# Performance work log

Hardware: AMD Instinct MI355X
Metric: run time of the kernel (lower is better)

Reference implementation:

```python
import jax, jax.numpy as jnp
import numpy as np

# Config from module init / global Args
H = 8        # n_head
DK = 64      # d_k
DV = 64      # d_v
D = 512      # d_model
KSZ = 3      # kernel_size (args.kernel_size)
B_PARAM = 0.001
CUR_HEAD = 3
ALPHA_C = -float(np.log(B_PARAM / (H - 1) * CUR_HEAD))  # alpha_c (nonzero head)
EPS = 1e-6


def setup_inputs() -> dict:
    key = jax.random.key(0)
    ks = jax.random.split(key, 8)
    B, L = 2, 2048
    q = jax.random.normal(ks[0], (B, L, D), jnp.float32)
    k = jax.random.normal(ks[1], (B, L, D), jnp.float32)
    v = jax.random.normal(ks[2], (B, L, D), jnp.float32)
    # Linear weights stored torch-style: [out_features, in_features]
    w_q = jax.random.normal(ks[3], (H * DK, D), jnp.float32) * 0.02
    w_k = jax.random.normal(ks[4], (H * DK, D), jnp.float32) * 0.02
    w_v = jax.random.normal(ks[5], (H * DV, D), jnp.float32) * 0.02
    w_fc = jax.random.normal(ks[6], (D, H * DV), jnp.float32) * 0.02
    gamma = jnp.ones((D,), jnp.float32)
    beta = jnp.zeros((D,), jnp.float32)
    return {"q": q, "k": k, "v": v, "w_q": w_q, "w_k": w_k, "w_v": w_v,
            "w_fc": w_fc, "gamma": gamma, "beta": beta}


def reference(q, k, v, w_q, w_k, w_v, w_fc, gamma, beta):
    B, L, _ = q.shape
    residual = q
    # QKV projections -> [B, H, L, d]
    qh = jnp.einsum('bld,ed->ble', q, w_q).reshape(B, L, H, DK).transpose(0, 2, 1, 3)
    kh = jnp.einsum('bld,ed->ble', k, w_k).reshape(B, L, H, DK).transpose(0, 2, 1, 3)
    vh = jnp.einsum('bld,ed->ble', v, w_v).reshape(B, L, H, DV).transpose(0, 2, 1, 3)
    # Scores: matmul(q / sqrt(d_k), k^T)  (LaSAttention receives d_k = d_k**0.5)
    attn = jnp.einsum('bhqd,bhkd->bhqk', qh, kh) / jnp.sqrt(jnp.float32(DK))
    # Distance weighting: eld = alpha_c * -(x - y) * attn, d_l[i,j] = j - i
    idx = jnp.arange(L)
    d_l = idx[None, :] - idx[:, None]                      # [L, L]
    eld_mat = (-ALPHA_C * d_l).astype(attn.dtype)
    eld = eld_mat[None, None, :, :] * attn
    # Softmax then avg_pool1d(kernel=KSZ, stride=1, pad=(KSZ-1)//2, count_include_pad)
    p = jax.nn.softmax(eld, axis=-1)                       # [B, H, L, L]
    pad = (KSZ - 1) // 2
    pp = jnp.pad(p, ((0, 0), (0, 0), (0, 0), (pad, pad)))
    pooled = sum(pp[..., j:j + L] for j in range(KSZ)) / jnp.float32(KSZ)
    # Value matmul (seq lengths equal so no trimming needed)
    out = jnp.einsum('bhqk,bhkd->bhqd', pooled, vh)
    out = out.transpose(0, 2, 1, 3).reshape(B, L, H * DV)
    # Output projection (dropout is identity in eval), residual, LayerNorm
    out = jnp.einsum('ble,de->bld', out, w_fc)
    out = out[:, :, None, :] + residual[:, :, None, :]     # [B, L, 1, D]
    mu = out.mean(axis=-1, keepdims=True)
    var = ((out - mu) ** 2).mean(axis=-1, keepdims=True)
    out = (out - mu) / jnp.sqrt(var + EPS) * gamma + beta
    return (out, pooled)
```

## Files before the change

kernel.cpp:

```cpp
#include <hip/hip_runtime.h>
#include <cstddef>
#include <cstdint>

#define ALPHA_C 7.7550531393693407f
constexpr int BB = 2;
constexpr int LL = 2048;
constexpr int HH = 8;
constexpr size_t OUT0  = (size_t)BB * LL * 512;
constexpr size_t PLANE = (size_t)BB * HH * LL * 64;
constexpr size_t XN    = (size_t)BB * LL * 512;
constexpr size_t WN    = (size_t)512 * 512;
constexpr size_t UN    = (size_t)16 * 32 * 32 * 4096;

typedef __attribute__((ext_vector_type(8))) short bf16x8;
typedef __attribute__((ext_vector_type(4))) short short4v;
typedef __attribute__((ext_vector_type(4))) float f32x4;

__device__ inline short f2bf(float x) {
  union { float f; unsigned u; } un; un.f = x;
  unsigned r = un.u + 0x7fffu + ((un.u >> 16) & 1u);
  return (short)(r >> 16);
}
__device__ inline float bf2f(short s) {
  union { unsigned u; float f; } un; un.u = ((unsigned)(unsigned short)s) << 16;
  return un.f;
}
__device__ inline void split3(float x, short& h, short& m, short& l) {
  h = f2bf(x); float r = x - bf2f(h);
  m = f2bf(r); float r2 = r - bf2f(m);
  l = f2bf(r2);
}

__global__ __launch_bounds__(256) void k_split3x(
    const float* __restrict__ a, const float* __restrict__ b, const float* __restrict__ c,
    short* __restrict__ da, short* __restrict__ db, short* __restrict__ dc, size_t n)
{
  size_t i = ((size_t)blockIdx.x * 256 + threadIdx.x) * 4;
  if (i >= n) return;
  const float* srcs[3] = {a, b, c};
  short* dsts[3] = {da, db, dc};
  #pragma unroll
  for (int s = 0; s < 3; ++s) {
    float4 x = *(const float4*)&srcs[s][i];
    short4v h, m, l;
    short th, tm, tl;
    split3(x.x, th, tm, tl); h[0] = th; m[0] = tm; l[0] = tl;
    split3(x.y, th, tm, tl); h[1] = th; m[1] = tm; l[1] = tl;
    split3(x.z, th, tm, tl); h[2] = th; m[2] = tm; l[2] = tl;
    split3(x.w, th, tm, tl); h[3] = th; m[3] = tm; l[3] = tl;
    *(short4v*)&dsts[s][i]         = h;
    *(short4v*)&dsts[s][n + i]     = m;
    *(short4v*)&dsts[s][2 * n + i] = l;
  }
}

__global__ __launch_bounds__(256) void k_cvtbf(
    const float* __restrict__ src, short* __restrict__ dst, size_t n)
{
  size_t i = ((size_t)blockIdx.x * 256 + threadIdx.x) * 8;
  if (i >= n) return;
  float4 a = *(const float4*)&src[i];
  float4 b = *(const float4*)&src[i + 4];
  bf16x8 o;
  o[0] = f2bf(a.x); o[1] = f2bf(a.y); o[2] = f2bf(a.z); o[3] = f2bf(a.w);
  o[4] = f2bf(b.x); o[5] = f2bf(b.y); o[6] = f2bf(b.z); o[7] = f2bf(b.w);
  *(bf16x8*)&dst[i] = o;
}

__global__ __launch_bounds__(256) void k_vavg(
    const short* __restrict__ vt, short* __restrict__ vavgt)
{
  const size_t row = blockIdx.x;
  const short* src = vt + row * LL;
  short* dst = vavgt + row * LL;
  const int c0 = threadIdx.x * 8;
  bf16x8 x = *(const bf16x8*)&src[c0];
  float xf[10];
  xf[0] = (c0 > 0) ? bf2f(src[c0 - 1]) : 0.f;
  #pragma unroll
  for (int i = 0; i < 8; ++i) xf[i + 1] = bf2f(x[i]);
  xf[9] = (c0 + 8 < LL) ? bf2f(src[c0 + 8]) : 0.f;
  bf16x8 o;
  #pragma unroll
  for (int i = 0; i < 8; ++i) o[i] = f2bf((xf[i] + xf[i + 1] + xf[i + 2]) * (1.0f / 3.0f));
  *(bf16x8*)&dst[c0] = o;
}

__global__ __launch_bounds__(256) void k_proj(
    const short* __restrict__ xq, const short* __restrict__ xk, const short* __restrict__ xv,
    const short* __restrict__ wq3, const short* __restrict__ wk3, const short* __restrict__ wv3,
    short* __restrict__ qs, short* __restrict__ ks, short* __restrict__ vt)
{
  const int bx  = blockIdx.x;
  const int sel = bx >> 3;
  const int n0  = (bx & 7) * 64;
  const int m0  = blockIdx.y * 64;
  const short* X = sel == 0 ? xq  : (sel == 1 ? xk  : xv);
  const short* W = sel == 0 ? wq3 : (sel == 1 ? wk3 : wv3);

  __shared__ short Xs[3][64 * 72];
  __shared__ short Ws[3][64 * 72];
  const int tid = threadIdx.x;
  const int lane = tid & 63, w = tid >> 6;
  const int quad = lane >> 4, l15 = lane & 15, colg = l15;
  const int sr8 = tid >> 3, sc8 = (tid & 7) * 8;

  f32x4 acc[4];
  #pragma unroll
  for (int t = 0; t < 4; ++t) { acc[t][0]=0.f; acc[t][1]=0.f; acc[t][2]=0.f; acc[t][3]=0.f; }

  for (int kt = 0; kt < 8; ++kt) {
    const int k0 = kt * 64;
    #pragma unroll
    for (int p = 0; p < 3; ++p) {
      #pragma unroll
      for (int it = 0; it < 2; ++it) {
        int r = it * 32 + sr8;
        *(bf16x8*)&Xs[p][r * 72 + sc8] = *(const bf16x8*)&X[p * XN + (size_t)(m0 + r) * 512 + k0 + sc8];
        *(bf16x8*)&Ws[p][r * 72 + sc8] = *(const bf16x8*)&W[p * WN + (size_t)(n0 + r) * 512 + k0 + sc8];
      }
    }
    __syncthreads();
    #pragma unroll
    for (int ch = 0; ch < 2; ++ch) {
      const int ka = (quad << 3) + ch * 32;
      const int ar = (w * 16 + l15) * 72 + ka;
      bf16x8 ah = *(const bf16x8*)&Xs[0][ar];
      bf16x8 am = *(const bf16x8*)&Xs[1][ar];
      bf16x8 al = *(const bf16x8*)&Xs[2][ar];
      #pragma unroll
      for (int t = 0; t < 4; ++t) {
        const int br = (t * 16 + l15) * 72 + ka;
        bf16x8 bh_ = *(const bf16x8*)&Ws[0][br];
        bf16x8 bm_ = *(const bf16x8*)&Ws[1][br];
        bf16x8 bl_ = *(const bf16x8*)&Ws[2][br];
        acc[t] = __builtin_amdgcn_mfma_f32_16x16x32_bf16(ah, bh_, acc[t], 0, 0, 0);
        acc[t] = __builtin_amdgcn_mfma_f32_16x16x32_bf16(ah, bm_, acc[t], 0, 0, 0);
        acc[t] = __builtin_amdgcn_mfma_f32_16x16x32_bf16(am, bh_, acc[t], 0, 0, 0);
        acc[t] = __builtin_amdgcn_mfma_f32_16x16x32_bf16(ah, bl_, acc[t], 0, 0, 0);
        acc[t] = __builtin_amdgcn_mfma_f32_16x16x32_bf16(al, bh_, acc[t], 0, 0, 0);
        acc[t] = __builtin_amdgcn_mfma_f32_16x16x32_bf16(am, bm_, acc[t], 0, 0, 0);
      }
    }
    __syncthreads();
  }

  if (sel < 2) {
    short* Y = sel == 0 ? qs : ks;
    #pragma unroll
    for (int t = 0; t < 4; ++t) {
      const int e = n0 + t * 16 + colg, h = e >> 6, dk = e & 63;
      #pragma unroll
      for (int r = 0; r < 4; ++r) {
        const int m = m0 + w * 16 + quad * 4 + r;
        const int b = m >> 11, l = m & 2047;
        size_t base = ((size_t)(b * HH + h) * LL + l) * 64 + dk;
        short hh, mm, ll; split3(acc[t][r], hh, mm, ll);
        Y[base] = hh; Y[PLANE + base] = mm; Y[2 * PLANE + base] = ll;
      }
    }
  } else {
    const int b  = m0 >> 11;
    const int l0 = (m0 & 2047) + w * 16 + quad * 4;
    #pragma unroll
    for (int t = 0; t < 4; ++t) {
      const int e = n0 + t * 16 + colg, h = e >> 6, dk = e & 63;
      short4v s;
      #pragma unroll
      for (int r = 0; r < 4; ++r) s[r] = f2bf(acc[t][r]);
      *(short4v*)&vt[(((size_t)b * HH + h) * 64 + dk) * LL + l0] = s;
    }
  }
}

__global__ __launch_bounds__(256) void k_qk_exp(
    const short* __restrict__ qs, const short* __restrict__ ks,
    short* __restrict__ u_g, float* __restrict__ mstats, float* __restrict__ rowstats)
{
  const int i0 = blockIdx.x * 64;
  const int bh = blockIdx.y;
  __shared__ short Ks[3][64 * 72];
  __shared__ short Us[64 * 72];
  const int tid = threadIdx.x;
  const int lane = tid & 63, w = tid >> 6;
  const int quad = lane >> 4, colg = lane & 15, l15 = lane & 15;
  const int sr8 = tid >> 3, sc8 = (tid & 7) * 8;

  bf16x8 qf[3][2];
  {
    const size_t qoff = ((size_t)bh * LL + i0 + w * 16 + l15) * 64 + (quad << 3);
    #pragma unroll
    for (int p = 0; p < 3; ++p)
      #pragma unroll
      for (int ch = 0; ch < 2; ++ch)
        qf[p][ch] = *(const bf16x8*)&qs[p * PLANE + qoff + ch * 32];
  }

  const short* kbase = ks + (size_t)bh * LL * 64;
  #pragma unroll
  for (int p = 0; p < 3; ++p)
    #pragma unroll
    for (int it = 0; it < 2; ++it) {
      int r = it * 32 + sr8;
      *(bf16x8*)&Ks[p][r * 72 + sc8] = *(const bf16x8*)&kbase[p * PLANE + (size_t)r * 64 + sc8];
    }
  __syncthreads();

  float M[4], S[4];
  #pragma unroll
  for (int r = 0; r < 4; ++r) { M[r] = -3.0e38f; S[r] = 0.f; }

  for (int jt = 0; jt < 32; ++jt) {
    const int j0 = jt * 64;
    bf16x8 kreg[3][2];
    if (jt + 1 < 32) {
      #pragma unroll
      for (int p = 0; p < 3; ++p)
        #pragma unroll
        for (int it = 0; it < 2; ++it) {
          int r = it * 32 + sr8;
          kreg[p][it] = *(const bf16x8*)&kbase[p * PLANE + ((size_t)(jt + 1) * 64 + r) * 64 + sc8];
        }
    }

    f32x4 acc[4];
    #pragma unroll
    for (int t = 0; t < 4; ++t) { acc[t][0]=0.f; acc[t][1]=0.f; acc[t][2]=0.f; acc[t][3]=0.f; }
    #pragma unroll
    for (int ch = 0; ch < 2; ++ch) {
      const int ka = (quad << 3) + ch * 32;
      #pragma unroll
      for (int t = 0; t < 4; ++t) {
        const int br = (t * 16 + l15) * 72 + ka;
        bf16x8 bh_ = *(const bf16x8*)&Ks[0][br];
        bf16x8 bm_ = *(const bf16x8*)&Ks[1][br];
        bf16x8 bl_ = *(const bf16x8*)&Ks[2][br];
        acc[t] = __builtin_amdgcn_mfma_f32_16x16x32_bf16(qf[0][ch], bh_, acc[t], 0, 0, 0);
        acc[t] = __builtin_amdgcn_mfma_f32_16x16x32_bf16(qf[0][ch], bm_, acc[t], 0, 0, 0);
        acc[t] = __builtin_amdgcn_mfma_f32_16x16x32_bf16(qf[1][ch], bh_, acc[t], 0, 0, 0);
        acc[t] = __builtin_amdgcn_mfma_f32_16x16x32_bf16(qf[0][ch], bl_, acc[t], 0, 0, 0);
        acc[t] = __builtin_amdgcn_mfma_f32_16x16x32_bf16(qf[2][ch], bh_, acc[t], 0, 0, 0);
        acc[t] = __builtin_amdgcn_mfma_f32_16x16x32_bf16(qf[1][ch], bm_, acc[t], 0, 0, 0);
      }
    }

    #pragma unroll
    for (int r = 0; r < 4; ++r) {
      const int row = w * 16 + quad * 4 + r;
      const int irow = i0 + row;
      float e0 = -ALPHA_C * (float)(j0 +  0 + colg - irow) * (acc[0][r] * 0.125f);
      float e1 = -ALPHA_C * (float)(j0 + 16 + colg - irow) * (acc[1][r] * 0.125f);
      float e2 = -ALPHA_C * (float)(j0 + 32 + colg - irow) * (acc[2][r] * 0.125f);
      float e3 = -ALPHA_C * (float)(j0 + 48 + colg - irow) * (acc[3][r] * 0.125f);
      float mx = fmaxf(fmaxf(e0, e1), fmaxf(e2, e3));
      #pragma unroll
      for (int d = 1; d < 16; d <<= 1) mx = fmaxf(mx, __shfl_xor(mx, d));
      float u0 = __expf(e0 - mx), u1 = __expf(e1 - mx);
      float u2 = __expf(e2 - mx), u3 = __expf(e3 - mx);
      float s = u0 + u1 + u2 + u3;
      #pragma unroll
      for (int d = 1; d < 16; d <<= 1) s += __shfl_xor(s, d);
      float nM = fmaxf(M[r], mx);
      S[r] = S[r] * __expf(M[r] - nM) + s * __expf(mx - nM);
      M[r] = nM;
      Us[row * 72 +  0 + colg] = f2bf(u0);
      Us[row * 72 + 16 + colg] = f2bf(u1);
      Us[row * 72 + 32 + colg] = f2bf(u2);
      Us[row * 72 + 48 + colg] = f2bf(u3);
      if (colg == 0) mstats[((size_t)bh * 32 + jt) * LL + irow] = mx;
    }
    __syncthreads();

    if (jt + 1 < 32) {
      #pragma unroll
      for (int p = 0; p < 3; ++p)
        #pragma unroll
        for (int it = 0; it < 2; ++it) {
          int r = it * 32 + sr8;
          *(bf16x8*)&Ks[p][r * 72 + sc8] = kreg[p][it];
        }
    }
    {
      const size_t ubase = (((size_t)bh * 32 + blockIdx.x) * 32 + jt) * 4096;
      #pragma unroll
      for (int it = 0; it < 2; ++it) {
        int rr = it * 32 + sr8;
        bf16x8 uu = *(const bf16x8*)&Us[rr * 72 + sc8];
        *(bf16x8*)&u_g[ubase + (size_t)rr * 64 + sc8] = uu;
      }
    }
    __syncthreads();
  }

  if (colg == 0) {
    #pragma unroll
    for (int r = 0; r < 4; ++r) {
      int irow = i0 + w * 16 + quad * 4 + r;
      size_t idx = ((size_t)bh * LL + irow) * 2;
      rowstats[idx] = M[r]; rowstats[idx + 1] = S[r];
    }
  }
}

__global__ __launch_bounds__(256) void k_pv2(
    const short* __restrict__ u_g, const float* __restrict__ mstats,
    const short* __restrict__ vavgt, const float* __restrict__ rowstats,
    float* __restrict__ pooled, short* __restrict__ outh)
{
  const int i0 = blockIdx.x * 64, ib = blockIdx.x;
  const int bh = blockIdx.y;
  const int b = bh >> 3, h = bh & 7;
  float*       Pg = pooled + (size_t)bh * LL * LL;
  const short* Vt = vavgt + (size_t)bh * 64 * LL;

  __shared__ short Vsm[64 * 72];
  __shared__ short Pa[2][64 * 72];
  __shared__ float lhalo[64];

  const int tid = threadIdx.x;
  const int lane = tid & 63, w = tid >> 6;
  const int quad = lane >> 4, colg = lane & 15, l15 = lane & 15;
  const int sr8 = tid >> 3, sc8 = (tid & 7) * 8;

  const int r0 = sr8, r1 = sr8 + 32;
  float M0, iS0, M1, iS1;
  {
    float2 a = *(const float2*)&rowstats[((size_t)bh * LL + i0 + r0) * 2];
    float2 c = *(const float2*)&rowstats[((size_t)bh * LL + i0 + r1) * 2];
    M0 = a.x; iS0 = 1.0f / a.y; M1 = c.x; iS1 = 1.0f / c.y;
  }
  if (tid < 64) lhalo[tid] = 0.f;
  __syncthreads();

  f32x4 pv[4];
  #pragma unroll
  for (int t = 0; t < 4; ++t) { pv[t][0]=0.f; pv[t][1]=0.f; pv[t][2]=0.f; pv[t][3]=0.f; }

  for (int jt = 0; jt <= 32; ++jt) {
    if (jt < 32) {
      const size_t ubase = (((size_t)bh * 32 + ib) * 32 + jt) * 4096;
      const float* mst = &mstats[((size_t)bh * 32 + jt) * LL + i0];
      float c0 = __expf(mst[r0] - M0) * iS0;
      float c1 = __expf(mst[r1] - M1) * iS1;
      bf16x8 u0 = *(const bf16x8*)&u_g[ubase + (size_t)r0 * 64 + sc8];
      bf16x8 u1 = *(const bf16x8*)&u_g[ubase + (size_t)r1 * 64 + sc8];
      bf16x8 p0, p1;
      #pragma unroll
      for (int i = 0; i < 8; ++i) {
        p0[i] = f2bf(bf2f(u0[i]) * c0);
        p1[i] = f2bf(bf2f(u1[i]) * c1);
      }
      *(bf16x8*)&Pa[jt & 1][r0 * 72 + sc8] = p0;
      *(bf16x8*)&Pa[jt & 1][r1 * 72 + sc8] = p1;
    }
    if (jt >= 1) {
      #pragma unroll
      for (int it = 0; it < 2; ++it) {
        int d = it * 32 + sr8;
        *(bf16x8*)&Vsm[d * 72 + sc8] = *(const bf16x8*)&Vt[(size_t)d * LL + (jt - 1) * 64 + sc8];
      }
    }
    __syncthreads();

    if (jt >= 1) {
      const short* Pp = Pa[(jt - 1) & 1];
      const short* Pn = Pa[jt & 1];
      #pragma unroll
      for (int u = 0; u < 2; ++u) {
        const int row = (u == 0) ? (tid >> 3) : (tid >> 3) + 32;
        const int c0 = (tid & 7) * 8;
        bf16x8 x = *(const bf16x8*)&Pp[row * 72 + c0];
        float xf[8];
        #pragma unroll
        for (int i = 0; i < 8; ++i) xf[i] = bf2f(x[i]);
        float lft = (c0 == 0)  ? lhalo[row] : bf2f(Pp[row * 72 + c0 - 1]);
        float rgt = (c0 == 56) ? ((jt < 32) ? bf2f(Pn[row * 72]) : 0.f)
                               : bf2f(Pp[row * 72 + c0 + 8]);
        f32x4 o0, o1;
        o0[0] = (lft   + xf[0] + xf[1]) * (1.0f/3.0f);
        o0[1] = (xf[0] + xf[1] + xf[2]) * (1.0f/3.0f);
        o0[2] = (xf[1] + xf[2] + xf[3]) * (1.0f/3.0f);
        o0[3] = (xf[2] + xf[3] + xf[4]) * (1.0f/3.0f);
        o1[0] = (xf[3] + xf[4] + xf[5]) * (1.0f/3.0f);
        o1[1] = (xf[4] + xf[5] + xf[6]) * (1.0f/3.0f);
        o1[2] = (xf[5] + xf[6] + xf[7]) * (1.0f/3.0f);
        o1[3] = (xf[6] + xf[7] + rgt  ) * (1.0f/3.0f);
        float* dst = &Pg[(size_t)(i0 + row) * LL + (jt - 1) * 64 + c0];
        __builtin_nontemporal_store(o0, (f32x4*)dst);
        __builtin_nontemporal_store(o1, (f32x4*)(dst + 4));
        if (c0 == 56) lhalo[row] = xf[7];
      }
      #pragma unroll
      for (int ch = 0; ch < 2; ++ch) {
        const int ka = (quad << 3) + ch * 32;
        bf16x8 af = *(const bf16x8*)&Pp[(w * 16 + l15) * 72 + ka];
        #pragma unroll
        for (int t = 0; t < 4; ++t) {
          bf16x8 bfv = *(const bf16x8*)&Vsm[(t * 16 + l15) * 72 + ka];
          pv[t] = __builtin_amdgcn_mfma_f32_16x16x32_bf16(af, bfv, pv[t], 0, 0, 0);
        }
      }
    }
    __syncthreads();
  }

  #pragma unroll
  for (int t = 0; t < 4; ++t)
    #pragma unroll
    for (int r = 0; r < 4; ++r) {
      int i = i0 + w * 16 + quad * 4 + r;
      int d = t * 16 + colg;
      outh[((size_t)b * LL + i) * 512 + h * 64 + d] = f2bf(pv[t][r]);
    }
}

__global__ __launch_bounds__(256) void k_fc(
    const short* __restrict__ outh, const short* __restrict__ wfcb, float* __restrict__ fcout)
{
  const int n0 = blockIdx.x * 64;
  const int m0 = blockIdx.y * 64;
  __shared__ short Asm[64 * 72];
  __shared__ short Bsm[64 * 72];
  const int tid = threadIdx.x;
  const int lane = tid & 63, w = tid >> 6;
  const int sr8 = tid >> 3, sc8 = (tid & 7) * 8;

  f32x4 acc[4];
  #pragma unroll
  for (int t = 0; t < 4; ++t) { acc[t][0]=0.f; acc[t][1]=0.f; acc[t][2]=0.f; acc[t][3]=0.f; }

  for (int k0 = 0; k0 < 512; k0 += 64) {
    #pragma unroll
    for (int it = 0; it < 2; ++it) {
      int r = it * 32 + sr8;
      *(bf16x8*)&Asm[r * 72 + sc8] = *(const bf16x8*)&outh[(size_t)(m0 + r) * 512 + k0 + sc8];
      *(bf16x8*)&Bsm[r * 72 + sc8] = *(const bf16x8*)&wfcb[(size_t)(n0 + r) * 512 + k0 + sc8];
    }
    __syncthreads();
    #pragma unroll
    for (int ch = 0; ch < 2; ++ch) {
      const int ka = ((lane >> 4) << 3) + ch * 32;
      bf16x8 af = *(const bf16x8*)&Asm[(w * 16 + (lane & 15)) * 72 + ka];
      #pragma unroll
      for (int t = 0; t < 4; ++t) {
        bf16x8 bfv = *(const bf16x8*)&Bsm[(t * 16 + (lane & 15)) * 72 + ka];
        acc[t] = __builtin_amdgcn_mfma_f32_16x16x32_bf16(af, bfv, acc[t], 0, 0, 0);
      }
    }
    __syncthreads();
  }
  const int q4 = lane >> 4, colg = lane & 15;
  #pragma unroll
  for (int t = 0; t < 4; ++t)
    #pragma unroll
    for (int r = 0; r < 4; ++r) {
      int m = m0 + w * 16 + q4 * 4 + r;
      fcout[(size_t)m * 512 + n0 + t * 16 + colg] = acc[t][r];
    }
}

__global__ __launch_bounds__(256) void k_ln(
    const float* __restrict__ fcout, const float* __restrict__ resid,
    const float* __restrict__ gamma, const float* __restrict__ beta,
    float* __restrict__ out)
{
  const size_t row = blockIdx.x;
  const int tid = threadIdx.x;
  __shared__ float red[256];

  float x0 = fcout[row * 512 + tid]       + resid[row * 512 + tid];
  float x1 = fcout[row * 512 + 256 + tid] + resid[row * 512 + 256 + tid];

  red[tid] = x0 + x1; __syncthreads();
  for (int off = 128; off > 0; off >>= 1) {
    if (tid < off) red[tid] += red[tid + off];
    __syncthreads();
  }
  const float mu = red[0] * (1.0f / 512.0f); __syncthreads();

  float d0 = x0 - mu, d1 = x1 - mu;
  red[tid] = d0 * d0 + d1 * d1; __syncthreads();
  for (int off = 128; off > 0; off >>= 1) {
    if (tid < off) red[tid] += red[tid + off];
    __syncthreads();
  }
  const float var = red[0] * (1.0f / 512.0f);
  const float rstd = 1.0f / sqrtf(var + 1e-6f);

  out[row * 512 + tid]       = d0 * rstd * gamma[tid]       + beta[tid];
  out[row * 512 + 256 + tid] = d1 * rstd * gamma[tid + 256] + beta[tid + 256];
}

extern "C" void kernel_launch(void* const* d_in, const int* in_sizes, int n_in,
                              void* d_out, int out_size, void* d_ws, size_t ws_size,
                              hipStream_t stream)
{
  const float* q     = (const float*)d_in[0];
  const float* k     = (const float*)d_in[1];
  const float* v     = (const float*)d_in[2];
  const float* wq    = (const float*)d_in[3];
  const float* wk    = (const float*)d_in[4];
  const float* wv    = (const float*)d_in[5];
  const float* wfc   = (const float*)d_in[6];
  const float* gamma = (const float*)d_in[7];
  const float* beta  = (const float*)d_in[8];

  float* out    = (float*)d_out;
  float* pooled = out + OUT0;

  short* xq    = (short*)d_ws;
  short* xk    = xq + 3 * XN;
  short* xv    = xk + 3 * XN;
  short* wq3   = xv + 3 * XN;
  short* wk3   = wq3 + 3 * WN;
  short* wv3   = wk3 + 3 * WN;
  short* qsp   = wv3 + 3 * WN;
  short* ksp   = qsp + 3 * PLANE;
  short* vt    = ksp + 3 * PLANE;
  short* vavgt = vt + PLANE;
  short* wfcb  = vavgt + PLANE;
  short* outh  = wfcb + WN;
  short* u_g   = outh + OUT0;
  float* mstats   = (float*)(u_g + UN);
  float* rowstats = mstats + (size_t)16 * 32 * LL;
  float* fcout    = rowstats + 2 * (size_t)BB * HH * LL;

  k_split3x<<<dim3((unsigned)(XN / 4 / 256)), 256, 0, stream>>>(q, k, v, xq, xk, xv, XN);
  k_split3x<<<dim3((unsigned)(WN / 4 / 256)), 256, 0, stream>>>(wq, wk, wv, wq3, wk3, wv3, WN);
  k_cvtbf  <<<dim3((unsigned)(WN / 8 / 256)), 256, 0, stream>>>(wfc, wfcb, WN);
  k_proj   <<<dim3(24, 64), 256, 0, stream>>>(xq, xk, xv, wq3, wk3, wv3, qsp, ksp, vt);
  k_vavg   <<<dim3(1024),   256, 0, stream>>>(vt, vavgt);
  k_qk_exp <<<dim3(32, 16), 256, 0, stream>>>(qsp, ksp, u_g, mstats, rowstats);
  k_pv2    <<<dim3(32, 16), 256, 0, stream>>>(u_g, mstats, vavgt, rowstats, pooled, outh);
  k_fc     <<<dim3(8, 64),  256, 0, stream>>>(outh, wfcb, fcout);
  k_ln     <<<dim3(4096),   256, 0, stream>>>(fcout, q, gamma, beta, out);
}
```

Measured before the change: 573.0 us.

## Fuse P·V accumulation into QK-exp kernel with online-softmax rescaling

Moves the P·V matmul from the pooled-write kernel into the QK/exp kernel, flash-attention style. The output accumulator is rescaled each tile by the running max correction and divided by the row sum at the end. The second kernel now only reconstructs and writes the pooled probability matrix. This removes the per-tile V staging and MFMA work from the store-bound pooling kernel, at the cost of more registers and direct global V fragment loads in the QK kernel. It also changes numerics slightly, since P·V now uses unnormalized bf16 exponentials.

Result: slower. 606.0 us (+5.8%).

```diff
diff --git a/kernel.cpp b/kernel.cpp
--- a/kernel.cpp
+++ b/kernel.cpp
@@ -173,12 +173,15 @@
   }
 }
 
-__global__ __launch_bounds__(256) void k_qk_exp(
+__global__ __launch_bounds__(256) void k_flash(
     const short* __restrict__ qs, const short* __restrict__ ks,
-    short* __restrict__ u_g, float* __restrict__ mstats, float* __restrict__ rowstats)
+    const short* __restrict__ vavgt,
+    short* __restrict__ u_g, float* __restrict__ mstats, float* __restrict__ rowstats,
+    short* __restrict__ outh)
 {
   const int i0 = blockIdx.x * 64;
   const int bh = blockIdx.y;
+  const int b = bh >> 3, h = bh & 7;
   __shared__ short Ks[3][64 * 72];
   __shared__ short Us[64 * 72];
   const int tid = threadIdx.x;
@@ -197,6 +200,7 @@
   }
 
   const short* kbase = ks + (size_t)bh * LL * 64;
+  const short* Vt = vavgt + (size_t)bh * 64 * LL;
   #pragma unroll
   for (int p = 0; p < 3; ++p)
     #pragma unroll
@@ -209,6 +213,9 @@
   float M[4], S[4];
   #pragma unroll
   for (int r = 0; r < 4; ++r) { M[r] = -3.0e38f; S[r] = 0.f; }
+  f32x4 pv[4];
+  #pragma unroll
+  for (int t = 0; t < 4; ++t) { pv[t][0]=0.f; pv[t][1]=0.f; pv[t][2]=0.f; pv[t][3]=0.f; }
 
   for (int jt = 0; jt < 32; ++jt) {
     const int j0 = jt * 64;
@@ -222,6 +229,12 @@
           kreg[p][it] = *(const bf16x8*)&kbase[p * PLANE + ((size_t)(jt + 1) * 64 + r) * 64 + sc8];
         }
     }
+    bf16x8 vfrag[4][2];
+    #pragma unroll
+    for (int t = 0; t < 4; ++t)
+      #pragma unroll
+      for (int ch = 0; ch < 2; ++ch)
+        vfrag[t][ch] = *(const bf16x8*)&Vt[(size_t)(t * 16 + l15) * LL + j0 + (quad << 3) + ch * 32];
 
     f32x4 acc[4];
     #pragma unroll
@@ -244,6 +257,7 @@
       }
     }
 
+    float alf[4], bet[4];
     #pragma unroll
     for (int r = 0; r < 4; ++r) {
       const int row = w * 16 + quad * 4 + r;
@@ -261,7 +275,9 @@
       #pragma unroll
       for (int d = 1; d < 16; d <<= 1) s += __shfl_xor(s, d);
       float nM = fmaxf(M[r], mx);
-      S[r] = S[r] * __expf(M[r] - nM) + s * __expf(mx - nM);
+      alf[r] = __expf(M[r] - nM);
+      bet[r] = __expf(mx - nM);
+      S[r] = S[r] * alf[r] + s * bet[r];
       M[r] = nM;
       Us[row * 72 +  0 + colg] = f2bf(u0);
       Us[row * 72 + 16 + colg] = f2bf(u1);
@@ -271,6 +287,24 @@
     }
     __syncthreads();
 
+    {
+      f32x4 tmp[4];
+      #pragma unroll
+      for (int t = 0; t < 4; ++t) { tmp[t][0]=0.f; tmp[t][1]=0.f; tmp[t][2]=0.f; tmp[t][3]=0.f; }
+      #pragma unroll
+      for (int ch = 0; ch < 2; ++ch) {
+        bf16x8 af = *(const bf16x8*)&Us[(w * 16 + l15) * 72 + (quad << 3) + ch * 32];
+        #pragma unroll
+        for (int t = 0; t < 4; ++t)
+          tmp[t] = __builtin_amdgcn_mfma_f32_16x16x32_bf16(af, vfrag[t][ch], tmp[t], 0, 0, 0);
+      }
+      #pragma unroll
+      for (int t = 0; t < 4; ++t)
+        #pragma unroll
+        for (int r = 0; r < 4; ++r)
+          pv[t][r] = pv[t][r] * alf[r] + tmp[t][r] * bet[r];
+    }
+
     if (jt + 1 < 32) {
       #pragma unroll
       for (int p = 0; p < 3; ++p)
@@ -300,26 +334,29 @@
       rowstats[idx] = M[r]; rowstats[idx + 1] = S[r];
     }
   }
-}
-
-__global__ __launch_bounds__(256) void k_pv2(
+  #pragma unroll
+  for (int t = 0; t < 4; ++t)
+    #pragma unroll
+    for (int r = 0; r < 4; ++r) {
+      int i = i0 + w * 16 + quad * 4 + r;
+      int d = t * 16 + colg;
+      outh[((size_t)b * LL + i) * 512 + h * 64 + d] = f2bf(pv[t][r] / S[r]);
+    }
+}
+
+__global__ __launch_bounds__(256) void k_poolw(
     const short* __restrict__ u_g, const float* __restrict__ mstats,
-    const short* __restrict__ vavgt, const float* __restrict__ rowstats,
-    float* __restrict__ pooled, short* __restrict__ outh)
+    const float* __restrict__ rowstats, float* __restrict__ pooled)
 {
   const int i0 = blockIdx.x * 64, ib = blockIdx.x;
   const int bh = blockIdx.y;
-  const int b = bh >> 3, h = bh & 7;
-  float*       Pg = pooled + (size_t)bh * LL * LL;
-  const short* Vt = vavgt + (size_t)bh * 64 * LL;
-
-  __shared__ short Vsm[64 * 72];
+  float* Pg = pooled + (size_t)bh * LL * LL;
+
   __shared__ short Pa[2][64 * 72];
   __shared__ float lhalo[64];
 
   const int tid = threadIdx.x;
-  const int lane = tid & 63, w = tid >> 6;
-  const int quad = lane >> 4, colg = lane & 15, l15 = lane & 15;
+  const int w = tid >> 6;
   const int sr8 = tid >> 3, sc8 = (tid & 7) * 8;
 
   const int r0 = sr8, r1 = sr8 + 32;
@@ -331,10 +368,6 @@
   }
   if (tid < 64) lhalo[tid] = 0.f;
   __syncthreads();
-
-  f32x4 pv[4];
-  #pragma unroll
-  for (int t = 0; t < 4; ++t) { pv[t][0]=0.f; pv[t][1]=0.f; pv[t][2]=0.f; pv[t][3]=0.f; }
 
   for (int jt = 0; jt <= 32; ++jt) {
     if (jt < 32) {
@@ -353,13 +386,6 @@
       *(bf16x8*)&Pa[jt & 1][r0 * 72 + sc8] = p0;
       *(bf16x8*)&Pa[jt & 1][r1 * 72 + sc8] = p1;
     }
-    if (jt >= 1) {
-      #pragma unroll
-      for (int it = 0; it < 2; ++it) {
-        int d = it * 32 + sr8;
-        *(bf16x8*)&Vsm[d * 72 + sc8] = *(const bf16x8*)&Vt[(size_t)d * LL + (jt - 1) * 64 + sc8];
-      }
-    }
     __syncthreads();
 
     if (jt >= 1) {
@@ -367,8 +393,8 @@
       const short* Pn = Pa[jt & 1];
       #pragma unroll
       for (int u = 0; u < 2; ++u) {
-        const int row = (u == 0) ? (tid >> 3) : (tid >> 3) + 32;
-        const int c0 = (tid & 7) * 8;
+        const int row = (u == 0) ? r0 : r1;
+        const int c0 = sc8;
         bf16x8 x = *(const bf16x8*)&Pp[row * 72 + c0];
         float xf[8];
         #pragma unroll
@@ -390,28 +416,10 @@
         __builtin_nontemporal_store(o1, (f32x4*)(dst + 4));
         if (c0 == 56) lhalo[row] = xf[7];
       }
-      #pragma unroll
-      for (int ch = 0; ch < 2; ++ch) {
-        const int ka = (quad << 3) + ch * 32;
-        bf16x8 af = *(const bf16x8*)&Pp[(w * 16 + l15) * 72 + ka];
-        #pragma unroll
-        for (int t = 0; t < 4; ++t) {
-          bf16x8 bfv = *(const bf16x8*)&Vsm[(t * 16 + l15) * 72 + ka];
-          pv[t] = __builtin_amdgcn_mfma_f32_16x16x32_bf16(af, bfv, pv[t], 0, 0, 0);
-        }
-      }
-    }
-    __syncthreads();
-  }
-
-  #pragma unroll
-  for (int t = 0; t < 4; ++t)
-    #pragma unroll
-    for (int r = 0; r < 4; ++r) {
-      int i = i0 + w * 16 + quad * 4 + r;
-      int d = t * 16 + colg;
-      outh[((size_t)b * LL + i) * 512 + h * 64 + d] = f2bf(pv[t][r]);
-    }
+    }
+    __syncthreads();
+  }
+  (void)w;
 }
 
 __global__ __launch_bounds__(256) void k_fc(
@@ -530,8 +538,8 @@
   k_cvtbf  <<<dim3((unsigned)(WN / 8 / 256)), 256, 0, stream>>>(wfc, wfcb, WN);
   k_proj   <<<dim3(24, 64), 256, 0, stream>>>(xq, xk, xv, wq3, wk3, wv3, qsp, ksp, vt);
   k_vavg   <<<dim3(1024),   256, 0, stream>>>(vt, vavgt);
-  k_qk_exp <<<dim3(32, 16), 256, 0, stream>>>(qsp, ksp, u_g, mstats, rowstats);
-  k_pv2    <<<dim3(32, 16), 256, 0, stream>>>(u_g, mstats, vavgt, rowstats, pooled, outh);
+  k_flash  <<<dim3(32, 16), 256, 0, stream>>>(qsp, ksp, vavgt, u_g, mstats, rowstats, outh);
+  k_poolw  <<<dim3(32, 16), 256, 0, stream>>>(u_g, mstats, rowstats, pooled);
   k_fc     <<<dim3(8, 64),  256, 0, stream>>>(outh, wfcb, fcout);
   k_ln     <<<dim3(4096),   256, 0, stream>>>(fcout, q, gamma, beta, out);
 }
```
